# Kernel optimization log

Hardware: AMD Instinct MI355X
Metric: run time of the kernel (lower is better)

Reference implementation:

```python
import math
import jax, jax.numpy as jnp
import numpy as np

B, T, D_MODEL, N_HEADS = 2, 2048, 1024, 16
HEAD_DIM = D_MODEL // N_HEADS  # 64


def setup_inputs() -> dict:
    key = jax.random.key(0)
    k1, k2, k3, k4, k5 = jax.random.split(key, 5)
    x = jax.random.normal(k1, (B, T, D_MODEL), dtype=jnp.float32)
    init = 0.02
    Wq = jax.random.normal(k2, (D_MODEL, D_MODEL), dtype=jnp.float32) * init
    Wk = jax.random.normal(k3, (D_MODEL, D_MODEL), dtype=jnp.float32) * init
    Wv = jax.random.normal(k4, (D_MODEL, D_MODEL), dtype=jnp.float32) * init
    Wo = jax.random.normal(k5, (D_MODEL, D_MODEL), dtype=jnp.float32) * init
    # causal mask, broadcastable over (B, H): 1 = keep, 0 = masked
    mask = jnp.tril(jnp.ones((T, T), dtype=jnp.int32))[None, None, :, :]
    return {"x": x, "Wq": Wq, "Wk": Wk, "Wv": Wv, "Wo": Wo, "mask": mask}


def ternary_weight(W):
    # BitNet-b1.58 style ternary quantization with straight-through estimator
    scale = jnp.mean(jnp.abs(W))
    Wt = jnp.round(jnp.clip(W / (scale + 1e-8), -1.0, 1.0)) * scale
    return W + jax.lax.stop_gradient(Wt - W)


def rope_cos_sin(seq_len, dim):
    inv_freq = 1.0 / (10000.0 ** (jnp.arange(0, dim, 2, dtype=jnp.float32) / dim))
    freqs = jnp.outer(jnp.arange(seq_len, dtype=jnp.float32), inv_freq)  # [T, dim/2]
    emb = jnp.concatenate([freqs, freqs], axis=-1)  # [T, dim]
    return jnp.cos(emb)[None, None, :, :], jnp.sin(emb)[None, None, :, :]


def rotate_half(x):
    h = x.shape[-1] // 2
    return jnp.concatenate([-x[..., h:], x[..., :h]], axis=-1)


def reference(x, Wq, Wk, Wv, Wo, mask):
    Bb, Tt, C = x.shape
    H, D = N_HEADS, HEAD_DIM
    # ternary-quantized projections (bias-free)
    q = (x @ ternary_weight(Wq).T).reshape(Bb, Tt, H, D).transpose(0, 2, 1, 3)
    k = (x @ ternary_weight(Wk).T).reshape(Bb, Tt, H, D).transpose(0, 2, 1, 3)
    v = (x @ ternary_weight(Wv).T).reshape(Bb, Tt, H, D).transpose(0, 2, 1, 3)
    cos, sin = rope_cos_sin(Tt, D)  # [1,1,T,D]
    q = q * cos + rotate_half(q) * sin
    k = k * cos + rotate_half(k) * sin
    att = jnp.einsum("bhqd,bhkd->bhqk", q, k) / math.sqrt(D)
    att = jnp.where(mask == 0, -jnp.inf, att)
    att = jax.nn.softmax(att, axis=-1)  # dropout omitted (eval mode, p effectively 0)
    y = jnp.einsum("bhqk,bhkd->bhqd", att, v)
    y = y.transpose(0, 2, 1, 3).reshape(Bb, Tt, C)
    return y @ ternary_weight(Wo).T
```

## Files before the change

### kernel.cpp

```cpp
#include <hip/hip_runtime.h>
#include <math.h>

using bf16x8  = __attribute__((ext_vector_type(8))) __bf16;
using floatx4 = __attribute__((ext_vector_type(4))) float;
using ushortx8 = __attribute__((ext_vector_type(8))) unsigned short;
typedef unsigned short u16;

__device__ __forceinline__ float bf2f(u16 u) {
  unsigned int x = ((unsigned int)u) << 16;
  return __builtin_bit_cast(float, x);
}
__device__ __forceinline__ u16 f2bf(float f) {
  unsigned int x = __builtin_bit_cast(unsigned int, f);
  x += 0x7FFFu + ((x >> 16) & 1u);
  return (u16)(x >> 16);
}
__device__ __forceinline__ float fexp2(float x) { return __builtin_amdgcn_exp2f(x); }
__device__ __forceinline__ unsigned cvtpk(float lo, float hi) {
  unsigned r;
  asm("v_cvt_pk_bf16_f32 %0, %1, %2" : "=v"(r) : "v"(lo), "v"(hi));
  return r;
}

__global__ __launch_bounds__(256) void cvt_kernel(const float* __restrict__ x, u16* __restrict__ xb) {
  int g = (blockIdx.x * 256 + threadIdx.x) * 8;
  float4 a = *(const float4*)(x + g);
  float4 b = *(const float4*)(x + g + 4);
  ushortx8 o;
  o[0] = f2bf(a.x); o[1] = f2bf(a.y); o[2] = f2bf(a.z); o[3] = f2bf(a.w);
  o[4] = f2bf(b.x); o[5] = f2bf(b.y); o[6] = f2bf(b.z); o[7] = f2bf(b.w);
  *(ushortx8*)(xb + g) = o;
}

__global__ __launch_bounds__(256) void absum_kernel(const float* W0, const float* W1,
                                                    const float* W2, const float* W3,
                                                    float* partials) {
  const float* W = (blockIdx.y == 0) ? W0 : (blockIdx.y == 1) ? W1 : (blockIdx.y == 2) ? W2 : W3;
  int tid = threadIdx.x;
  int base = blockIdx.x * 16384 + tid;
  float s = 0.f;
#pragma unroll
  for (int i = 0; i < 64; ++i) s += fabsf(W[base + i * 256]);
  __shared__ float red[256];
  red[tid] = s;
  __syncthreads();
  for (int off = 128; off > 0; off >>= 1) {
    if (tid < off) red[tid] += red[tid + off];
    __syncthreads();
  }
  if (tid == 0) partials[blockIdx.y * 64 + blockIdx.x] = red[0];
}

__global__ void scales_kernel(const float* partials, float* scales) {
  int w = threadIdx.x;
  if (w < 4) {
    float s = 0.f;
    for (int i = 0; i < 64; ++i) s += partials[w * 64 + i];
    scales[w] = s * (1.f / 1048576.f);
  }
}

__global__ __launch_bounds__(256) void quant_kernel(const float* W0, const float* W1,
                                                    const float* W2, const float* W3,
                                                    const float* scales, u16* Wt) {
  int w = blockIdx.y;
  const float* W = (w == 0) ? W0 : (w == 1) ? W1 : (w == 2) ? W2 : W3;
  u16* O = Wt + (size_t)w * (1u << 20);
  float s = scales[w] + 1e-8f;
  int e = blockIdx.x * 256 + threadIdx.x;
  float t = W[e] / s;
  t = fminf(fmaxf(t, -1.f), 1.f);
  O[e] = f2bf(rintf(t));
}

__global__ __launch_bounds__(256) void gemm_qkv(const u16* __restrict__ A, const u16* __restrict__ Wt,
                                                u16* __restrict__ QKV, const float* __restrict__ scales) {
  const int K = 1024;
  __shared__ __align__(16) u16 As[128][64];
  __shared__ __align__(16) u16 Bs[128][64];
  int tid = threadIdx.x;
  int wave = tid >> 6, lane = tid & 63;
  int quad = lane >> 4, l16 = lane & 15;
  int bm = blockIdx.x * 128;
  int bnc = blockIdx.y * 128;
  int mat = bnc >> 10, bn = bnc & 1023;
  int wm = (wave >> 1) * 64, wn = (wave & 1) * 64;
  floatx4 acc[4][4] = {};
  const u16* ga = A  + (size_t)(bm + wave * 32 + (lane >> 3)) * K + (lane & 7) * 8;
  const u16* gb = Wt + (size_t)(bnc + wave * 32 + (lane >> 3)) * K + (lane & 7) * 8;
  for (int k0 = 0; k0 < K; k0 += 64) {
    __syncthreads();
#pragma unroll
    for (int i = 0; i < 4; ++i)
      __builtin_amdgcn_global_load_lds(
          (const __attribute__((address_space(1))) void*)(ga + (size_t)i * 8 * K + k0),
          (__attribute__((address_space(3))) void*)(&As[wave * 32 + i * 8][0]), 16, 0, 0);
#pragma unroll
    for (int i = 0; i < 4; ++i)
      __builtin_amdgcn_global_load_lds(
          (const __attribute__((address_space(1))) void*)(gb + (size_t)i * 8 * K + k0),
          (__attribute__((address_space(3))) void*)(&Bs[wave * 32 + i * 8][0]), 16, 0, 0);
    __syncthreads();
#pragma unroll
    for (int kk = 0; kk < 64; kk += 32) {
      bf16x8 a[4], b[4];
#pragma unroll
      for (int i = 0; i < 4; ++i)
        a[i] = __builtin_bit_cast(bf16x8, *(const ushortx8*)&As[wm + i * 16 + l16][kk + quad * 8]);
#pragma unroll
      for (int j = 0; j < 4; ++j)
        b[j] = __builtin_bit_cast(bf16x8, *(const ushortx8*)&Bs[wn + j * 16 + l16][kk + quad * 8]);
#pragma unroll
      for (int i = 0; i < 4; ++i)
#pragma unroll
        for (int j = 0; j < 4; ++j)
          acc[i][j] = __builtin_amdgcn_mfma_f32_16x16x32_bf16(a[i], b[j], acc[i][j], 0, 0, 0);
    }
  }
  float sc = scales[mat];
  u16* out = QKV + (size_t)mat * (4u << 20);
#pragma unroll
  for (int i = 0; i < 4; ++i)
#pragma unroll
    for (int j = 0; j < 4; ++j)
#pragma unroll
      for (int rg = 0; rg < 4; ++rg) {
        int row = bm + wm + i * 16 + quad * 4 + rg;
        int col = bn + wn + j * 16 + l16;
        out[(size_t)row * 1024 + col] = f2bf(acc[i][j][rg] * sc);
      }
}

__global__ __launch_bounds__(256) void gemm_out(const u16* __restrict__ A, const u16* __restrict__ B,
                                                float* __restrict__ C, const float* __restrict__ scale_ptr) {
  const int K = 1024, N = 1024;
  __shared__ __align__(16) u16 As[128][64];
  __shared__ __align__(16) u16 Bs[128][64];
  int tid = threadIdx.x;
  int wave = tid >> 6, lane = tid & 63;
  int quad = lane >> 4, l16 = lane & 15;
  int bm = blockIdx.x * 128, bn = blockIdx.y * 128;
  int wm = (wave >> 1) * 64, wn = (wave & 1) * 64;
  floatx4 acc[4][4] = {};
  const u16* ga = A + (size_t)(bm + wave * 32 + (lane >> 3)) * K + (lane & 7) * 8;
  const u16* gb = B + (size_t)(bn + wave * 32 + (lane >> 3)) * K + (lane & 7) * 8;
  for (int k0 = 0; k0 < K; k0 += 64) {
    __syncthreads();
#pragma unroll
    for (int i = 0; i < 4; ++i)
      __builtin_amdgcn_global_load_lds(
          (const __attribute__((address_space(1))) void*)(ga + (size_t)i * 8 * K + k0),
          (__attribute__((address_space(3))) void*)(&As[wave * 32 + i * 8][0]), 16, 0, 0);
#pragma unroll
    for (int i = 0; i < 4; ++i)
      __builtin_amdgcn_global_load_lds(
          (const __attribute__((address_space(1))) void*)(gb + (size_t)i * 8 * K + k0),
          (__attribute__((address_space(3))) void*)(&Bs[wave * 32 + i * 8][0]), 16, 0, 0);
    __syncthreads();
#pragma unroll
    for (int kk = 0; kk < 64; kk += 32) {
      bf16x8 a[4], b[4];
#pragma unroll
      for (int i = 0; i < 4; ++i)
        a[i] = __builtin_bit_cast(bf16x8, *(const ushortx8*)&As[wm + i * 16 + l16][kk + quad * 8]);
#pragma unroll
      for (int j = 0; j < 4; ++j)
        b[j] = __builtin_bit_cast(bf16x8, *(const ushortx8*)&Bs[wn + j * 16 + l16][kk + quad * 8]);
#pragma unroll
      for (int i = 0; i < 4; ++i)
#pragma unroll
        for (int j = 0; j < 4; ++j)
          acc[i][j] = __builtin_amdgcn_mfma_f32_16x16x32_bf16(a[i], b[j], acc[i][j], 0, 0, 0);
    }
  }
  float sc = scale_ptr[0];
#pragma unroll
  for (int i = 0; i < 4; ++i)
#pragma unroll
    for (int j = 0; j < 4; ++j)
#pragma unroll
      for (int rg = 0; rg < 4; ++rg) {
        int row = bm + wm + i * 16 + quad * 4 + rg;
        int col = bn + wn + j * 16 + l16;
        C[(size_t)row * N + col] = acc[i][j][rg] * sc;
      }
}

__global__ __launch_bounds__(256) void rope_kernel(u16* q, u16* k) {
  const float QS = 0.125f * 1.4426950408889634f;
  int gid = blockIdx.x * 256 + threadIdx.x;
  int i = gid & 31;
  int h = (gid >> 5) & 15;
  int bt = gid >> 9;
  int t = bt & 2047;
  float inv = exp2f(-(float)i * (13.287712379549449f / 32.f));
  float ang = (float)t * inv;
  float s = __sinf(ang), c = __cosf(ang);
  int row = bt * 1024 + h * 64;
  float q1 = bf2f(q[row + i]), q2 = bf2f(q[row + i + 32]);
  q[row + i]      = f2bf((q1 * c - q2 * s) * QS);
  q[row + i + 32] = f2bf((q2 * c + q1 * s) * QS);
  float k1 = bf2f(k[row + i]), k2 = bf2f(k[row + i + 32]);
  k[row + i]      = f2bf(k1 * c - k2 * s);
  k[row + i + 32] = f2bf(k2 * c + k1 * s);
}

__global__ __launch_bounds__(256) void vtrans_kernel(const u16* __restrict__ v, u16* __restrict__ vt) {
  __shared__ u16 L[64][66];
  int bh = blockIdx.y, b = bh >> 4, h = bh & 15;
  int t0 = blockIdx.x * 64;
  int tid = threadIdx.x;
  int r = tid >> 2, c = (tid & 3) << 4;
  const u16* src = v + (size_t)(b * 2048 + t0 + r) * 1024 + h * 64 + c;
  *(ushortx8*)&L[r][c]     = *(const ushortx8*)src;
  *(ushortx8*)&L[r][c + 8] = *(const ushortx8*)(src + 8);
  __syncthreads();
  int d = tid >> 2, tc = (tid & 3) << 4;
  ushortx8 o0, o1;
#pragma unroll
  for (int j = 0; j < 8; ++j) { o0[j] = L[tc + j][d]; o1[j] = L[tc + 8 + j][d]; }
  u16* dst = vt + (size_t)(bh * 64 + d) * 2048 + t0 + tc;
  *(ushortx8*)dst       = o0;
  *(ushortx8*)(dst + 8) = o1;
}

__global__ __launch_bounds__(256, 2) void attn_kernel(const u16* __restrict__ q, const u16* __restrict__ k,
                                                      const u16* __restrict__ vt, u16* __restrict__ y) {
  __shared__ __align__(16) u16 Ks[2][64][72];
  __shared__ __align__(16) u16 Vt[2][64][72];
  __shared__ __align__(16) u16 Ps[8][16][72];
  const int T = 2048, C = 1024;
  int tid = threadIdx.x;
  int wave = tid >> 6, lane = tid & 63;
  int quad = lane >> 4, l16 = lane & 15;
  int p = blockIdx.x;
  int b = blockIdx.y >> 4, h = blockIdx.y & 15;
  int wq[2];
  wq[0] = p * 64 + wave * 16;
  wq[1] = (31 - p) * 64 + wave * 16;
  int dt[2] = {p, 31 - p};
  int nkt = 32 - p;

  bf16x8 bq[2][2];
#pragma unroll
  for (int g = 0; g < 2; ++g) {
    const u16* gq = q + (size_t)(b * T + wq[g] + l16) * C + h * 64 + quad * 8;
    bq[g][0] = __builtin_bit_cast(bf16x8, *(const ushortx8*)(gq));
    bq[g][1] = __builtin_bit_cast(bf16x8, *(const ushortx8*)(gq + 32));
  }

  ushortx8 onesu;
#pragma unroll
  for (int j = 0; j < 8; ++j) onesu[j] = 0x3F80;
  bf16x8 bones = __builtin_bit_cast(bf16x8, onesu);

  int srow = tid >> 2, sc16 = (tid & 3) << 4;
  const u16* kptr  = k  + (size_t)(b * T + srow) * C + h * 64 + sc16;
  const u16* vtptr = vt + (size_t)(blockIdx.y * 64 + srow) * 2048 + sc16;

  floatx4 o[2][5] = {};

  ushortx8 kra = *(const ushortx8*)kptr;
  ushortx8 krb = *(const ushortx8*)(kptr + 8);
  ushortx8 vra = *(const ushortx8*)vtptr;
  ushortx8 vrb = *(const ushortx8*)(vtptr + 8);
  *(ushortx8*)&Ks[0][srow][sc16]     = kra;
  *(ushortx8*)&Ks[0][srow][sc16 + 8] = krb;
  *(ushortx8*)&Vt[0][srow][sc16]     = vra;
  *(ushortx8*)&Vt[0][srow][sc16 + 8] = vrb;
  __syncthreads();

  for (int kt = 0; kt < nkt; ++kt) {
    int cur = kt & 1;
    bool haveNext = (kt + 1) < nkt;
    if (haveNext) {
      kra = *(const ushortx8*)(kptr + (size_t)(kt + 1) * 64 * C);
      krb = *(const ushortx8*)(kptr + (size_t)(kt + 1) * 64 * C + 8);
      vra = *(const ushortx8*)(vtptr + (kt + 1) * 64);
      vrb = *(const ushortx8*)(vtptr + (kt + 1) * 64 + 8);
    }

    bool act[2] = {kt <= dt[0], true};

    floatx4 sacc[2][4] = {};
#pragma unroll
    for (int nt = 0; nt < 4; ++nt) {
      bf16x8 ak0 = __builtin_bit_cast(bf16x8, *(const ushortx8*)&Ks[cur][nt * 16 + l16][quad * 8]);
      bf16x8 ak1 = __builtin_bit_cast(bf16x8, *(const ushortx8*)&Ks[cur][nt * 16 + l16][32 + quad * 8]);
#pragma unroll
      for (int g = 0; g < 2; ++g)
        if (act[g]) {
          sacc[g][nt] = __builtin_amdgcn_mfma_f32_16x16x32_bf16(ak0, bq[g][0], sacc[g][nt], 0, 0, 0);
          sacc[g][nt] = __builtin_amdgcn_mfma_f32_16x16x32_bf16(ak1, bq[g][1], sacc[g][nt], 0, 0, 0);
        }
    }

#pragma unroll
    for (int g = 0; g < 2; ++g)
      if (act[g]) {
        if (kt == dt[g]) {
          int qg = wq[g] + l16;
#pragma unroll
          for (int nt = 0; nt < 4; ++nt)
#pragma unroll
            for (int rg = 0; rg < 4; ++rg)
              if (kt * 64 + nt * 16 + quad * 4 + rg > qg) sacc[g][nt][rg] = -__builtin_inff();
        }
#pragma unroll
        for (int nt = 0; nt < 4; ++nt) {
          float p0 = fexp2(sacc[g][nt][0]);
          float p1 = fexp2(sacc[g][nt][1]);
          float p2 = fexp2(sacc[g][nt][2]);
          float p3 = fexp2(sacc[g][nt][3]);
          unsigned lo = cvtpk(p0, p1);
          unsigned hi = cvtpk(p2, p3);
          *(uint2*)&Ps[wave * 2 + g][l16][nt * 16 + quad * 4] = make_uint2(lo, hi);
        }
      }

    bf16x8 ap[2][2];
#pragma unroll
    for (int g = 0; g < 2; ++g)
      if (act[g]) {
        ap[g][0] = __builtin_bit_cast(bf16x8, *(const ushortx8*)&Ps[wave * 2 + g][l16][quad * 8]);
        ap[g][1] = __builtin_bit_cast(bf16x8, *(const ushortx8*)&Ps[wave * 2 + g][l16][32 + quad * 8]);
      }
#pragma unroll
    for (int nt = 0; nt < 4; ++nt) {
      bf16x8 bv0 = __builtin_bit_cast(bf16x8, *(const ushortx8*)&Vt[cur][nt * 16 + l16][quad * 8]);
      bf16x8 bv1 = __builtin_bit_cast(bf16x8, *(const ushortx8*)&Vt[cur][nt * 16 + l16][32 + quad * 8]);
#pragma unroll
      for (int g = 0; g < 2; ++g)
        if (act[g]) {
          o[g][nt] = __builtin_amdgcn_mfma_f32_16x16x32_bf16(ap[g][0], bv0, o[g][nt], 0, 0, 0);
          o[g][nt] = __builtin_amdgcn_mfma_f32_16x16x32_bf16(ap[g][1], bv1, o[g][nt], 0, 0, 0);
        }
    }
#pragma unroll
    for (int g = 0; g < 2; ++g)
      if (act[g]) {
        o[g][4] = __builtin_amdgcn_mfma_f32_16x16x32_bf16(ap[g][0], bones, o[g][4], 0, 0, 0);
        o[g][4] = __builtin_amdgcn_mfma_f32_16x16x32_bf16(ap[g][1], bones, o[g][4], 0, 0, 0);
      }

    if (haveNext) {
      int nb = cur ^ 1;
      *(ushortx8*)&Ks[nb][srow][sc16]     = kra;
      *(ushortx8*)&Ks[nb][srow][sc16 + 8] = krb;
      *(ushortx8*)&Vt[nb][srow][sc16]     = vra;
      *(ushortx8*)&Vt[nb][srow][sc16 + 8] = vrb;
    }
    __syncthreads();
  }

#pragma unroll
  for (int g = 0; g < 2; ++g)
#pragma unroll
    for (int nt = 0; nt < 4; ++nt)
#pragma unroll
      for (int rg = 0; rg < 4; ++rg) {
        int qg = wq[g] + quad * 4 + rg;
        int col = h * 64 + nt * 16 + l16;
        y[(size_t)(b * T + qg) * C + col] = f2bf(o[g][nt][rg] / o[g][4][rg]);
      }
}

extern "C" void kernel_launch(void* const* d_in, const int* in_sizes, int n_in,
                              void* d_out, int out_size, void* d_ws, size_t ws_size,
                              hipStream_t stream) {
  const float* x  = (const float*)d_in[0];
  const float* Wq = (const float*)d_in[1];
  const float* Wk = (const float*)d_in[2];
  const float* Wv = (const float*)d_in[3];
  const float* Wo = (const float*)d_in[4];

  char* ws = (char*)d_ws;
  float* partials = (float*)ws;
  float* scales   = (float*)(ws + 1024);
  u16* Wt  = (u16*)(ws + 4096);
  u16* xb  = (u16*)(ws + 4096 + (size_t)(8u << 20));
  u16* qb  = xb + (4u << 20);
  u16* kb  = qb + (4u << 20);
  u16* vb  = kb + (4u << 20);
  u16* vtb = vb + (4u << 20);
  u16* yb  = vtb + (4u << 20);
  float* out = (float*)d_out;

  cvt_kernel<<<2048, 256, 0, stream>>>(x, xb);
  absum_kernel<<<dim3(64, 4), 256, 0, stream>>>(Wq, Wk, Wv, Wo, partials);
  scales_kernel<<<1, 64, 0, stream>>>(partials, scales);
  quant_kernel<<<dim3(4096, 4), 256, 0, stream>>>(Wq, Wk, Wv, Wo, scales, Wt);

  gemm_qkv<<<dim3(32, 24), 256, 0, stream>>>(xb, Wt, qb, scales);
  rope_kernel<<<8192, 256, 0, stream>>>(qb, kb);
  vtrans_kernel<<<dim3(32, 32), 256, 0, stream>>>(vb, vtb);
  attn_kernel<<<dim3(16, 32), 256, 0, stream>>>(qb, kb, vtb, yb);
  gemm_out<<<dim3(32, 8), 256, 0, stream>>>(yb, Wt + 3 * (1u << 20), out, scales + 3);
}
```

Before: 227.1 us.

## Fuse RoPE into QKV GEMM epilogue, double-buffer and swizzle GEMM LDS tiles

The RoPE rotation and the Q scaling move into the QKV GEMM epilogue. Each wave's 64-column tile covers one full head, so element pairs (d, d+32) sit in the accumulators j and j+2. This removes the separate rope kernel and its read-modify-write pass over Q and K. Both GEMMs switch to a BK=32 double-buffered LDS pipeline with XOR-swizzled columns to cut bank conflicts and overlap loads with MFMA. The output GEMM tile is halved to 128x64 so the grid has 512 blocks for better occupancy, at the cost of less data reuse per block.

```diff
diff --git a/kernel.cpp b/kernel.cpp
--- a/kernel.cpp
+++ b/kernel.cpp
@@ -76,8 +76,8 @@
 __global__ __launch_bounds__(256) void gemm_qkv(const u16* __restrict__ A, const u16* __restrict__ Wt,
                                                 u16* __restrict__ QKV, const float* __restrict__ scales) {
   const int K = 1024;
-  __shared__ __align__(16) u16 As[128][64];
-  __shared__ __align__(16) u16 Bs[128][64];
+  __shared__ __align__(16) u16 As[2][128][32];
+  __shared__ __align__(16) u16 Bs[2][128][32];
   int tid = threadIdx.x;
   int wave = tid >> 6, lane = tid & 63;
   int quad = lane >> 4, l16 = lane & 15;
@@ -86,123 +86,153 @@
   int mat = bnc >> 10, bn = bnc & 1023;
   int wm = (wave >> 1) * 64, wn = (wave & 1) * 64;
   floatx4 acc[4][4] = {};
-  const u16* ga = A  + (size_t)(bm + wave * 32 + (lane >> 3)) * K + (lane & 7) * 8;
-  const u16* gb = Wt + (size_t)(bnc + wave * 32 + (lane >> 3)) * K + (lane & 7) * 8;
-  for (int k0 = 0; k0 < K; k0 += 64) {
+  int srow = wave * 16 + (lane >> 2);
+  int scol = ((lane & 3) ^ ((lane >> 3) & 3)) * 8;
+  const u16* ga = A  + (size_t)(bm + srow) * K + scol;
+  const u16* gb = Wt + (size_t)(bnc + srow) * K + scol;
+  int rca = (quad ^ ((l16 >> 1) & 3)) * 8;
+
+#pragma unroll
+  for (int i = 0; i < 2; ++i) {
+    __builtin_amdgcn_global_load_lds(
+        (const __attribute__((address_space(1))) void*)(ga + (size_t)i * 64 * K),
+        (__attribute__((address_space(3))) void*)(&As[0][i * 64 + wave * 16][0]), 16, 0, 0);
+    __builtin_amdgcn_global_load_lds(
+        (const __attribute__((address_space(1))) void*)(gb + (size_t)i * 64 * K),
+        (__attribute__((address_space(3))) void*)(&Bs[0][i * 64 + wave * 16][0]), 16, 0, 0);
+  }
+  __syncthreads();
+
+  for (int k0 = 0; k0 < K; k0 += 32) {
+    int cur = (k0 >> 5) & 1;
+    if (k0 + 32 < K) {
+      int nb = cur ^ 1;
+#pragma unroll
+      for (int i = 0; i < 2; ++i) {
+        __builtin_amdgcn_global_load_lds(
+            (const __attribute__((address_space(1))) void*)(ga + (size_t)i * 64 * K + k0 + 32),
+            (__attribute__((address_space(3))) void*)(&As[nb][i * 64 + wave * 16][0]), 16, 0, 0);
+        __builtin_amdgcn_global_load_lds(
+            (const __attribute__((address_space(1))) void*)(gb + (size_t)i * 64 * K + k0 + 32),
+            (__attribute__((address_space(3))) void*)(&Bs[nb][i * 64 + wave * 16][0]), 16, 0, 0);
+      }
+    }
+    bf16x8 a[4], b[4];
+#pragma unroll
+    for (int i = 0; i < 4; ++i)
+      a[i] = __builtin_bit_cast(bf16x8, *(const ushortx8*)&As[cur][wm + i * 16 + l16][rca]);
+#pragma unroll
+    for (int j = 0; j < 4; ++j)
+      b[j] = __builtin_bit_cast(bf16x8, *(const ushortx8*)&Bs[cur][wn + j * 16 + l16][rca]);
+#pragma unroll
+    for (int i = 0; i < 4; ++i)
+#pragma unroll
+      for (int j = 0; j < 4; ++j)
+        acc[i][j] = __builtin_amdgcn_mfma_f32_16x16x32_bf16(a[i], b[j], acc[i][j], 0, 0, 0);
     __syncthreads();
-#pragma unroll
-    for (int i = 0; i < 4; ++i)
-      __builtin_amdgcn_global_load_lds(
-          (const __attribute__((address_space(1))) void*)(ga + (size_t)i * 8 * K + k0),
-          (__attribute__((address_space(3))) void*)(&As[wave * 32 + i * 8][0]), 16, 0, 0);
-#pragma unroll
-    for (int i = 0; i < 4; ++i)
-      __builtin_amdgcn_global_load_lds(
-          (const __attribute__((address_space(1))) void*)(gb + (size_t)i * 8 * K + k0),
-          (__attribute__((address_space(3))) void*)(&Bs[wave * 32 + i * 8][0]), 16, 0, 0);
-    __syncthreads();
-#pragma unroll
-    for (int kk = 0; kk < 64; kk += 32) {
-      bf16x8 a[4], b[4];
-#pragma unroll
-      for (int i = 0; i < 4; ++i)
-        a[i] = __builtin_bit_cast(bf16x8, *(const ushortx8*)&As[wm + i * 16 + l16][kk + quad * 8]);
-#pragma unroll
-      for (int j = 0; j < 4; ++j)
-        b[j] = __builtin_bit_cast(bf16x8, *(const ushortx8*)&Bs[wn + j * 16 + l16][kk + quad * 8]);
-#pragma unroll
-      for (int i = 0; i < 4; ++i)
-#pragma unroll
-        for (int j = 0; j < 4; ++j)
-          acc[i][j] = __builtin_amdgcn_mfma_f32_16x16x32_bf16(a[i], b[j], acc[i][j], 0, 0, 0);
-    }
-  }
+  }
+
   float sc = scales[mat];
   u16* out = QKV + (size_t)mat * (4u << 20);
-#pragma unroll
-  for (int i = 0; i < 4; ++i)
-#pragma unroll
-    for (int j = 0; j < 4; ++j)
+  if (mat < 2) {
+    float qs = (mat == 0) ? 0.125f * 1.4426950408889634f : 1.0f;
+    float inv0 = exp2f(-(float)l16 * (13.287712379549449f / 32.f));
+    float inv1 = exp2f(-(float)(16 + l16) * (13.287712379549449f / 32.f));
+#pragma unroll
+    for (int i = 0; i < 4; ++i)
 #pragma unroll
       for (int rg = 0; rg < 4; ++rg) {
         int row = bm + wm + i * 16 + quad * 4 + rg;
-        int col = bn + wn + j * 16 + l16;
-        out[(size_t)row * 1024 + col] = f2bf(acc[i][j][rg] * sc);
-      }
+        float tf = (float)(row & 2047);
+#pragma unroll
+        for (int j = 0; j < 2; ++j) {
+          float ang = tf * (j ? inv1 : inv0);
+          float s = __sinf(ang), c = __cosf(ang);
+          float v1 = acc[i][j][rg] * sc, v2 = acc[i][j + 2][rg] * sc;
+          int col = bn + wn + j * 16 + l16;
+          out[(size_t)row * 1024 + col]      = f2bf((v1 * c - v2 * s) * qs);
+          out[(size_t)row * 1024 + col + 32] = f2bf((v2 * c + v1 * s) * qs);
+        }
+      }
+  } else {
+#pragma unroll
+    for (int i = 0; i < 4; ++i)
+#pragma unroll
+      for (int j = 0; j < 4; ++j)
+#pragma unroll
+        for (int rg = 0; rg < 4; ++rg) {
+          int row = bm + wm + i * 16 + quad * 4 + rg;
+          int col = bn + wn + j * 16 + l16;
+          out[(size_t)row * 1024 + col] = f2bf(acc[i][j][rg] * sc);
+        }
+  }
 }
 
 __global__ __launch_bounds__(256) void gemm_out(const u16* __restrict__ A, const u16* __restrict__ B,
                                                 float* __restrict__ C, const float* __restrict__ scale_ptr) {
   const int K = 1024, N = 1024;
-  __shared__ __align__(16) u16 As[128][64];
-  __shared__ __align__(16) u16 Bs[128][64];
+  __shared__ __align__(16) u16 As[2][128][32];
+  __shared__ __align__(16) u16 Bs[2][64][32];
   int tid = threadIdx.x;
   int wave = tid >> 6, lane = tid & 63;
   int quad = lane >> 4, l16 = lane & 15;
-  int bm = blockIdx.x * 128, bn = blockIdx.y * 128;
-  int wm = (wave >> 1) * 64, wn = (wave & 1) * 64;
-  floatx4 acc[4][4] = {};
-  const u16* ga = A + (size_t)(bm + wave * 32 + (lane >> 3)) * K + (lane & 7) * 8;
-  const u16* gb = B + (size_t)(bn + wave * 32 + (lane >> 3)) * K + (lane & 7) * 8;
-  for (int k0 = 0; k0 < K; k0 += 64) {
+  int bm = blockIdx.x * 128, bn = blockIdx.y * 64;
+  int wm = (wave >> 1) * 64, wn = (wave & 1) * 32;
+  floatx4 acc[4][2] = {};
+  int srow = wave * 16 + (lane >> 2);
+  int scol = ((lane & 3) ^ ((lane >> 3) & 3)) * 8;
+  const u16* ga = A + (size_t)(bm + srow) * K + scol;
+  const u16* gb = B + (size_t)(bn + srow) * K + scol;
+  int rca = (quad ^ ((l16 >> 1) & 3)) * 8;
+
+#pragma unroll
+  for (int i = 0; i < 2; ++i)
+    __builtin_amdgcn_global_load_lds(
+        (const __attribute__((address_space(1))) void*)(ga + (size_t)i * 64 * K),
+        (__attribute__((address_space(3))) void*)(&As[0][i * 64 + wave * 16][0]), 16, 0, 0);
+  __builtin_amdgcn_global_load_lds(
+      (const __attribute__((address_space(1))) void*)(gb),
+      (__attribute__((address_space(3))) void*)(&Bs[0][wave * 16][0]), 16, 0, 0);
+  __syncthreads();
+
+  for (int k0 = 0; k0 < K; k0 += 32) {
+    int cur = (k0 >> 5) & 1;
+    if (k0 + 32 < K) {
+      int nb = cur ^ 1;
+#pragma unroll
+      for (int i = 0; i < 2; ++i)
+        __builtin_amdgcn_global_load_lds(
+            (const __attribute__((address_space(1))) void*)(ga + (size_t)i * 64 * K + k0 + 32),
+            (__attribute__((address_space(3))) void*)(&As[nb][i * 64 + wave * 16][0]), 16, 0, 0);
+      __builtin_amdgcn_global_load_lds(
+          (const __attribute__((address_space(1))) void*)(gb + k0 + 32),
+          (__attribute__((address_space(3))) void*)(&Bs[nb][wave * 16][0]), 16, 0, 0);
+    }
+    bf16x8 a[4], b[2];
+#pragma unroll
+    for (int i = 0; i < 4; ++i)
+      a[i] = __builtin_bit_cast(bf16x8, *(const ushortx8*)&As[cur][wm + i * 16 + l16][rca]);
+#pragma unroll
+    for (int j = 0; j < 2; ++j)
+      b[j] = __builtin_bit_cast(bf16x8, *(const ushortx8*)&Bs[cur][wn + j * 16 + l16][rca]);
+#pragma unroll
+    for (int i = 0; i < 4; ++i)
+#pragma unroll
+      for (int j = 0; j < 2; ++j)
+        acc[i][j] = __builtin_amdgcn_mfma_f32_16x16x32_bf16(a[i], b[j], acc[i][j], 0, 0, 0);
     __syncthreads();
-#pragma unroll
-    for (int i = 0; i < 4; ++i)
-      __builtin_amdgcn_global_load_lds(
-          (const __attribute__((address_space(1))) void*)(ga + (size_t)i * 8 * K + k0),
-          (__attribute__((address_space(3))) void*)(&As[wave * 32 + i * 8][0]), 16, 0, 0);
-#pragma unroll
-    for (int i = 0; i < 4; ++i)
-      __builtin_amdgcn_global_load_lds(
-          (const __attribute__((address_space(1))) void*)(gb + (size_t)i * 8 * K + k0),
-          (__attribute__((address_space(3))) void*)(&Bs[wave * 32 + i * 8][0]), 16, 0, 0);
-    __syncthreads();
-#pragma unroll
-    for (int kk = 0; kk < 64; kk += 32) {
-      bf16x8 a[4], b[4];
-#pragma unroll
-      for (int i = 0; i < 4; ++i)
-        a[i] = __builtin_bit_cast(bf16x8, *(const ushortx8*)&As[wm + i * 16 + l16][kk + quad * 8]);
-#pragma unroll
-      for (int j = 0; j < 4; ++j)
-        b[j] = __builtin_bit_cast(bf16x8, *(const ushortx8*)&Bs[wn + j * 16 + l16][kk + quad * 8]);
-#pragma unroll
-      for (int i = 0; i < 4; ++i)
-#pragma unroll
-        for (int j = 0; j < 4; ++j)
-          acc[i][j] = __builtin_amdgcn_mfma_f32_16x16x32_bf16(a[i], b[j], acc[i][j], 0, 0, 0);
-    }
   }
   float sc = scale_ptr[0];
 #pragma unroll
   for (int i = 0; i < 4; ++i)
 #pragma unroll
-    for (int j = 0; j < 4; ++j)
+    for (int j = 0; j < 2; ++j)
 #pragma unroll
       for (int rg = 0; rg < 4; ++rg) {
         int row = bm + wm + i * 16 + quad * 4 + rg;
         int col = bn + wn + j * 16 + l16;
         C[(size_t)row * N + col] = acc[i][j][rg] * sc;
       }
-}
-
-__global__ __launch_bounds__(256) void rope_kernel(u16* q, u16* k) {
-  const float QS = 0.125f * 1.4426950408889634f;
-  int gid = blockIdx.x * 256 + threadIdx.x;
-  int i = gid & 31;
-  int h = (gid >> 5) & 15;
-  int bt = gid >> 9;
-  int t = bt & 2047;
-  float inv = exp2f(-(float)i * (13.287712379549449f / 32.f));
-  float ang = (float)t * inv;
-  float s = __sinf(ang), c = __cosf(ang);
-  int row = bt * 1024 + h * 64;
-  float q1 = bf2f(q[row + i]), q2 = bf2f(q[row + i + 32]);
-  q[row + i]      = f2bf((q1 * c - q2 * s) * QS);
-  q[row + i + 32] = f2bf((q2 * c + q1 * s) * QS);
-  float k1 = bf2f(k[row + i]), k2 = bf2f(k[row + i + 32]);
-  k[row + i]      = f2bf(k1 * c - k2 * s);
-  k[row + i + 32] = f2bf(k2 * c + k1 * s);
 }
 
 __global__ __launch_bounds__(256) void vtrans_kernel(const u16* __restrict__ v, u16* __restrict__ vt) {
@@ -392,8 +422,7 @@
   quant_kernel<<<dim3(4096, 4), 256, 0, stream>>>(Wq, Wk, Wv, Wo, scales, Wt);
 
   gemm_qkv<<<dim3(32, 24), 256, 0, stream>>>(xb, Wt, qb, scales);
-  rope_kernel<<<8192, 256, 0, stream>>>(qb, kb);
   vtrans_kernel<<<dim3(32, 32), 256, 0, stream>>>(vb, vtb);
   attn_kernel<<<dim3(16, 32), 256, 0, stream>>>(qb, kb, vtb, yb);
-  gemm_out<<<dim3(32, 8), 256, 0, stream>>>(yb, Wt + 3 * (1u << 20), out, scales + 3);
-}
+  gemm_out<<<dim3(32, 16), 256, 0, stream>>>(yb, Wt + 3 * (1u << 20), out, scales + 3);
+}
```

Result: no change. 224.5 us (-1.1%).

## Rewrite QKV GEMM as 256x256 pipelined tile kernel and fuse RoPE epilogue

Applied to the files above, without the earlier changes.

The QKV projection GEMM becomes a 512-thread, 256x256-tile kernel. It double-buffers swizzled LDS tiles, interleaves global-to-LDS prefetch with MFMA phases using barriers and priority hints, and applies RoPE plus the q scaling directly in the epilogue. This lets the separate rope kernel and its extra read/write pass over Q and K be removed. The aim is better latency hiding and fewer bank conflicts in the dominant GEMM. The cost is a launch of only 192 blocks with heavier register and LDS use, plus a more fragile hand-tuned schedule.

```diff
diff --git a/kernel.cpp b/kernel.cpp
--- a/kernel.cpp
+++ b/kernel.cpp
@@ -21,6 +21,10 @@
   asm("v_cvt_pk_bf16_f32 %0, %1, %2" : "=v"(r) : "v"(lo), "v"(hi));
   return r;
 }
+
+#define GLDS16(SRC, DST)                                                        \
+  __builtin_amdgcn_global_load_lds((const __attribute__((address_space(1))) void*)(SRC), \
+                                   (__attribute__((address_space(3))) void*)(DST), 16, 0, 0)
 
 __global__ __launch_bounds__(256) void cvt_kernel(const float* __restrict__ x, u16* __restrict__ xb) {
   int g = (blockIdx.x * 256 + threadIdx.x) * 8;
@@ -73,62 +77,132 @@
   O[e] = f2bf(rintf(t));
 }
 
-__global__ __launch_bounds__(256) void gemm_qkv(const u16* __restrict__ A, const u16* __restrict__ Wt,
-                                                u16* __restrict__ QKV, const float* __restrict__ scales) {
-  const int K = 1024;
-  __shared__ __align__(16) u16 As[128][64];
-  __shared__ __align__(16) u16 Bs[128][64];
+__global__ __launch_bounds__(512, 2) void gemm_qkv(const u16* __restrict__ A, const u16* __restrict__ Wt,
+                                                   u16* __restrict__ QKV, const float* __restrict__ scales) {
+  const int K = 1024, NT = 16;
+  __shared__ __align__(16) u16 Ab[2][2][128][64];
+  __shared__ __align__(16) u16 Bb[2][2][128][64];
   int tid = threadIdx.x;
-  int wave = tid >> 6, lane = tid & 63;
+  int w = tid >> 6, lane = tid & 63;
   int quad = lane >> 4, l16 = lane & 15;
-  int bm = blockIdx.x * 128;
-  int bnc = blockIdx.y * 128;
+  int bm = blockIdx.x * 256;
+  int bnc = blockIdx.y * 256;
+  int halfA = w >> 2;
+  int halfB = (w & 3) >> 1;
+  int cbase = (w & 1) * 64;
+
+  int srow = w * 8 + (lane >> 3);
+  int scol = ((lane & 7) ^ (lane >> 3)) * 8;
+  const u16* gA = A  + (size_t)(bm  + srow) * K + scol;
+  const u16* gB = Wt + (size_t)(bnc + srow) * K + scol;
+
+#define STAGE(BUF, GP, PAR, HF, TAU)                                                    \
+  do {                                                                                  \
+    GLDS16(GP + (size_t)((HF) * 128) * 1024 + (size_t)(TAU) * 64, &BUF[PAR][HF][w * 8][0]); \
+    GLDS16(GP + (size_t)((HF) * 128 + 64) * 1024 + (size_t)(TAU) * 64, &BUF[PAR][HF][64 + w * 8][0]); \
+  } while (0)
+
+  floatx4 acc[8][4] = {};
+
+  STAGE(Ab, gA, 0, 0, 0); STAGE(Ab, gA, 0, 1, 0);
+  STAGE(Bb, gB, 0, 0, 0); STAGE(Bb, gB, 0, 1, 0);
+  STAGE(Bb, gB, 1, 0, 1); STAGE(Bb, gB, 1, 1, 1);
+  asm volatile("s_waitcnt vmcnt(4)" ::: "memory");
+  __builtin_amdgcn_s_barrier();
+
+  for (int it = 0; it < 8; ++it) {
+    int t = it * 2;
+    bf16x8 afr[4][2], bfr[2][2][2];
+#pragma unroll
+    for (int p = 0; p < 8; ++p) {
+      const int qd = p & 3, rh = qd >> 1, ch = qd & 1;
+      const int bb = (p >> 2) & 1;
+      if (ch == 0) {
+#pragma unroll
+        for (int i = 0; i < 4; ++i)
+#pragma unroll
+          for (int kk = 0; kk < 2; ++kk)
+            afr[i][kk] = __builtin_bit_cast(
+                bf16x8, *(const ushortx8*)&Ab[bb][halfA][rh * 64 + i * 16 + l16]
+                                             [((quad + kk * 4) ^ (l16 & 7)) * 8]);
+      }
+      if (rh == 0) {
+#pragma unroll
+        for (int gg = 0; gg < 2; ++gg)
+#pragma unroll
+          for (int kk = 0; kk < 2; ++kk)
+            bfr[ch][gg][kk] = __builtin_bit_cast(
+                bf16x8, *(const ushortx8*)&Bb[bb][halfB][cbase + ch * 32 + gg * 16 + l16]
+                                             [((quad + kk * 4) ^ (l16 & 7)) * 8]);
+      }
+      if (p == 0)      { STAGE(Ab, gA, 1, 0, t + 1); }
+      else if (p == 1) { STAGE(Ab, gA, 1, 1, t + 1); }
+      else if (p == 2) { if (it < 7) STAGE(Bb, gB, 0, 0, t + 2); }
+      else if (p == 3) { if (it < 7) STAGE(Bb, gB, 0, 1, t + 2); }
+      else if (p == 4) { if (it < 7) STAGE(Ab, gA, 0, 0, t + 2); }
+      else if (p == 5) { if (it < 7) STAGE(Ab, gA, 0, 1, t + 2); }
+      else if (p == 6) { if (it < 7) STAGE(Bb, gB, 1, 0, t + 3); }
+      else             { if (it < 7) STAGE(Bb, gB, 1, 1, t + 3); }
+
+      __builtin_amdgcn_s_barrier();
+      asm volatile("s_waitcnt lgkmcnt(0)" ::: "memory");
+      __builtin_amdgcn_sched_barrier(0);
+      __builtin_amdgcn_s_setprio(1);
+#pragma unroll
+      for (int i = 0; i < 4; ++i)
+#pragma unroll
+        for (int gg = 0; gg < 2; ++gg) {
+          acc[rh * 4 + i][ch * 2 + gg] = __builtin_amdgcn_mfma_f32_16x16x32_bf16(
+              afr[i][0], bfr[ch][gg][0], acc[rh * 4 + i][ch * 2 + gg], 0, 0, 0);
+          acc[rh * 4 + i][ch * 2 + gg] = __builtin_amdgcn_mfma_f32_16x16x32_bf16(
+              afr[i][1], bfr[ch][gg][1], acc[rh * 4 + i][ch * 2 + gg], 0, 0, 0);
+        }
+      __builtin_amdgcn_s_setprio(0);
+      if (qd == 3) {
+        if (it < 7) asm volatile("s_waitcnt vmcnt(4)" ::: "memory");
+        else        asm volatile("s_waitcnt vmcnt(0)" ::: "memory");
+      }
+      __builtin_amdgcn_s_barrier();
+      __builtin_amdgcn_sched_barrier(0);
+    }
+  }
+#undef STAGE
+
   int mat = bnc >> 10, bn = bnc & 1023;
-  int wm = (wave >> 1) * 64, wn = (wave & 1) * 64;
-  floatx4 acc[4][4] = {};
-  const u16* ga = A  + (size_t)(bm + wave * 32 + (lane >> 3)) * K + (lane & 7) * 8;
-  const u16* gb = Wt + (size_t)(bnc + wave * 32 + (lane >> 3)) * K + (lane & 7) * 8;
-  for (int k0 = 0; k0 < K; k0 += 64) {
-    __syncthreads();
-#pragma unroll
-    for (int i = 0; i < 4; ++i)
-      __builtin_amdgcn_global_load_lds(
-          (const __attribute__((address_space(1))) void*)(ga + (size_t)i * 8 * K + k0),
-          (__attribute__((address_space(3))) void*)(&As[wave * 32 + i * 8][0]), 16, 0, 0);
-#pragma unroll
-    for (int i = 0; i < 4; ++i)
-      __builtin_amdgcn_global_load_lds(
-          (const __attribute__((address_space(1))) void*)(gb + (size_t)i * 8 * K + k0),
-          (__attribute__((address_space(3))) void*)(&Bs[wave * 32 + i * 8][0]), 16, 0, 0);
-    __syncthreads();
-#pragma unroll
-    for (int kk = 0; kk < 64; kk += 32) {
-      bf16x8 a[4], b[4];
-#pragma unroll
-      for (int i = 0; i < 4; ++i)
-        a[i] = __builtin_bit_cast(bf16x8, *(const ushortx8*)&As[wm + i * 16 + l16][kk + quad * 8]);
-#pragma unroll
-      for (int j = 0; j < 4; ++j)
-        b[j] = __builtin_bit_cast(bf16x8, *(const ushortx8*)&Bs[wn + j * 16 + l16][kk + quad * 8]);
-#pragma unroll
-      for (int i = 0; i < 4; ++i)
-#pragma unroll
-        for (int j = 0; j < 4; ++j)
-          acc[i][j] = __builtin_amdgcn_mfma_f32_16x16x32_bf16(a[i], b[j], acc[i][j], 0, 0, 0);
-    }
-  }
   float sc = scales[mat];
-  u16* out = QKV + (size_t)mat * (4u << 20);
-#pragma unroll
-  for (int i = 0; i < 4; ++i)
-#pragma unroll
-    for (int j = 0; j < 4; ++j)
+  u16* outp = QKV + (size_t)mat * (4u << 20);
+  if (mat < 2) {
+    float qs = (mat == 0) ? 0.125f * 1.4426950408889634f : 1.0f;
+    float inv0 = exp2f(-(float)l16 * (13.287712379549449f / 32.f));
+    float inv1 = exp2f(-(float)(16 + l16) * (13.287712379549449f / 32.f));
+#pragma unroll
+    for (int f = 0; f < 8; ++f)
 #pragma unroll
       for (int rg = 0; rg < 4; ++rg) {
-        int row = bm + wm + i * 16 + quad * 4 + rg;
-        int col = bn + wn + j * 16 + l16;
-        out[(size_t)row * 1024 + col] = f2bf(acc[i][j][rg] * sc);
-      }
+        int row = bm + halfA * 128 + f * 16 + quad * 4 + rg;
+        float tf = (float)(row & 2047);
+#pragma unroll
+        for (int j = 0; j < 2; ++j) {
+          float ang = tf * (j ? inv1 : inv0);
+          float s = __sinf(ang), c = __cosf(ang);
+          float v1 = acc[f][j][rg] * sc, v2 = acc[f][j + 2][rg] * sc;
+          int col = bn + (w & 3) * 64 + j * 16 + l16;
+          outp[(size_t)row * 1024 + col]      = f2bf((v1 * c - v2 * s) * qs);
+          outp[(size_t)row * 1024 + col + 32] = f2bf((v2 * c + v1 * s) * qs);
+        }
+      }
+  } else {
+#pragma unroll
+    for (int f = 0; f < 8; ++f)
+#pragma unroll
+      for (int g = 0; g < 4; ++g)
+#pragma unroll
+        for (int rg = 0; rg < 4; ++rg) {
+          int row = bm + halfA * 128 + f * 16 + quad * 4 + rg;
+          int col = bn + (w & 3) * 64 + g * 16 + l16;
+          outp[(size_t)row * 1024 + col] = f2bf(acc[f][g][rg] * sc);
+        }
+  }
 }
 
 __global__ __launch_bounds__(256) void gemm_out(const u16* __restrict__ A, const u16* __restrict__ B,
@@ -148,14 +222,10 @@
     __syncthreads();
 #pragma unroll
     for (int i = 0; i < 4; ++i)
-      __builtin_amdgcn_global_load_lds(
-          (const __attribute__((address_space(1))) void*)(ga + (size_t)i * 8 * K + k0),
-          (__attribute__((address_space(3))) void*)(&As[wave * 32 + i * 8][0]), 16, 0, 0);
+      GLDS16(ga + (size_t)i * 8 * K + k0, &As[wave * 32 + i * 8][0]);
 #pragma unroll
     for (int i = 0; i < 4; ++i)
-      __builtin_amdgcn_global_load_lds(
-          (const __attribute__((address_space(1))) void*)(gb + (size_t)i * 8 * K + k0),
-          (__attribute__((address_space(3))) void*)(&Bs[wave * 32 + i * 8][0]), 16, 0, 0);
+      GLDS16(gb + (size_t)i * 8 * K + k0, &Bs[wave * 32 + i * 8][0]);
     __syncthreads();
 #pragma unroll
     for (int kk = 0; kk < 64; kk += 32) {
@@ -184,25 +254,6 @@
         int col = bn + wn + j * 16 + l16;
         C[(size_t)row * N + col] = acc[i][j][rg] * sc;
       }
-}
-
-__global__ __launch_bounds__(256) void rope_kernel(u16* q, u16* k) {
-  const float QS = 0.125f * 1.4426950408889634f;
-  int gid = blockIdx.x * 256 + threadIdx.x;
-  int i = gid & 31;
-  int h = (gid >> 5) & 15;
-  int bt = gid >> 9;
-  int t = bt & 2047;
-  float inv = exp2f(-(float)i * (13.287712379549449f / 32.f));
-  float ang = (float)t * inv;
-  float s = __sinf(ang), c = __cosf(ang);
-  int row = bt * 1024 + h * 64;
-  float q1 = bf2f(q[row + i]), q2 = bf2f(q[row + i + 32]);
-  q[row + i]      = f2bf((q1 * c - q2 * s) * QS);
-  q[row + i + 32] = f2bf((q2 * c + q1 * s) * QS);
-  float k1 = bf2f(k[row + i]), k2 = bf2f(k[row + i + 32]);
-  k[row + i]      = f2bf(k1 * c - k2 * s);
-  k[row + i + 32] = f2bf(k2 * c + k1 * s);
 }
 
 __global__ __launch_bounds__(256) void vtrans_kernel(const u16* __restrict__ v, u16* __restrict__ vt) {
@@ -391,8 +442,7 @@
   scales_kernel<<<1, 64, 0, stream>>>(partials, scales);
   quant_kernel<<<dim3(4096, 4), 256, 0, stream>>>(Wq, Wk, Wv, Wo, scales, Wt);
 
-  gemm_qkv<<<dim3(32, 24), 256, 0, stream>>>(xb, Wt, qb, scales);
-  rope_kernel<<<8192, 256, 0, stream>>>(qb, kb);
+  gemm_qkv<<<dim3(16, 12), 512, 0, stream>>>(xb, Wt, qb, scales);
   vtrans_kernel<<<dim3(32, 32), 256, 0, stream>>>(vb, vtb);
   attn_kernel<<<dim3(16, 32), 256, 0, stream>>>(qb, kb, vtb, yb);
   gemm_out<<<dim3(32, 8), 256, 0, stream>>>(yb, Wt + 3 * (1u << 20), out, scales + 3);
```

Result: faster. 212.8 us (-6.3%).

## Fuse RoPE and V transpose into QKV GEMM epilogue, vectorize quantization

Applied to the files above, without the earlier changes.

The QKV GEMM tile changes to 128x64 so that each block covers exactly one head. RoPE rotation and the Q scaling are then applied in the epilogue, and V is written directly in transposed layout. This removes the separate rope and vtrans kernels along with their global memory round trips. The block index is swizzled for L2 locality, and the quant kernel is vectorized to four elements per thread. In exchange, the epilogue does more per-element math and the transposed V stores are narrower.

```diff
diff --git a/kernel.cpp b/kernel.cpp
--- a/kernel.cpp
+++ b/kernel.cpp
@@ -4,6 +4,7 @@
 using bf16x8  = __attribute__((ext_vector_type(8))) __bf16;
 using floatx4 = __attribute__((ext_vector_type(4))) float;
 using ushortx8 = __attribute__((ext_vector_type(8))) unsigned short;
+using ushortx4 = __attribute__((ext_vector_type(4))) unsigned short;
 typedef unsigned short u16;
 
 __device__ __forceinline__ float bf2f(u16 u) {
@@ -21,6 +22,10 @@
   asm("v_cvt_pk_bf16_f32 %0, %1, %2" : "=v"(r) : "v"(lo), "v"(hi));
   return r;
 }
+
+#define GLDS16(SRC, DST)                                                        \
+  __builtin_amdgcn_global_load_lds((const __attribute__((address_space(1))) void*)(SRC), \
+                                   (__attribute__((address_space(3))) void*)(DST), 16, 0, 0)
 
 __global__ __launch_bounds__(256) void cvt_kernel(const float* __restrict__ x, u16* __restrict__ xb) {
   int g = (blockIdx.x * 256 + threadIdx.x) * 8;
@@ -67,68 +72,98 @@
   const float* W = (w == 0) ? W0 : (w == 1) ? W1 : (w == 2) ? W2 : W3;
   u16* O = Wt + (size_t)w * (1u << 20);
   float s = scales[w] + 1e-8f;
-  int e = blockIdx.x * 256 + threadIdx.x;
-  float t = W[e] / s;
-  t = fminf(fmaxf(t, -1.f), 1.f);
-  O[e] = f2bf(rintf(t));
+  int e = (blockIdx.x * 256 + threadIdx.x) * 4;
+  float4 v = *(const float4*)(W + e);
+  ushortx4 o;
+  o[0] = f2bf(rintf(fminf(fmaxf(v.x / s, -1.f), 1.f)));
+  o[1] = f2bf(rintf(fminf(fmaxf(v.y / s, -1.f), 1.f)));
+  o[2] = f2bf(rintf(fminf(fmaxf(v.z / s, -1.f), 1.f)));
+  o[3] = f2bf(rintf(fminf(fmaxf(v.w / s, -1.f), 1.f)));
+  *(ushortx4*)(O + e) = o;
 }
 
 __global__ __launch_bounds__(256) void gemm_qkv(const u16* __restrict__ A, const u16* __restrict__ Wt,
-                                                u16* __restrict__ QKV, const float* __restrict__ scales) {
+                                                u16* __restrict__ QKV, u16* __restrict__ vt,
+                                                const float* __restrict__ scales) {
   const int K = 1024;
   __shared__ __align__(16) u16 As[128][64];
-  __shared__ __align__(16) u16 Bs[128][64];
+  __shared__ __align__(16) u16 Bs[64][64];
   int tid = threadIdx.x;
   int wave = tid >> 6, lane = tid & 63;
   int quad = lane >> 4, l16 = lane & 15;
-  int bm = blockIdx.x * 128;
-  int bnc = blockIdx.y * 128;
+  int flat = blockIdx.y * 32 + blockIdx.x;
+  int swz = (flat & 7) * 192 + (flat >> 3);
+  int bx = swz & 31, by = swz >> 5;
+  int bm = bx * 128;
+  int bnc = by * 64;
   int mat = bnc >> 10, bn = bnc & 1023;
-  int wm = (wave >> 1) * 64, wn = (wave & 1) * 64;
-  floatx4 acc[4][4] = {};
+  int wm = wave * 32;
+  floatx4 acc[2][4] = {};
   const u16* ga = A  + (size_t)(bm + wave * 32 + (lane >> 3)) * K + (lane & 7) * 8;
-  const u16* gb = Wt + (size_t)(bnc + wave * 32 + (lane >> 3)) * K + (lane & 7) * 8;
+  const u16* gb = Wt + (size_t)(bnc + wave * 16 + (lane >> 3)) * K + (lane & 7) * 8;
   for (int k0 = 0; k0 < K; k0 += 64) {
     __syncthreads();
 #pragma unroll
     for (int i = 0; i < 4; ++i)
-      __builtin_amdgcn_global_load_lds(
-          (const __attribute__((address_space(1))) void*)(ga + (size_t)i * 8 * K + k0),
-          (__attribute__((address_space(3))) void*)(&As[wave * 32 + i * 8][0]), 16, 0, 0);
-#pragma unroll
-    for (int i = 0; i < 4; ++i)
-      __builtin_amdgcn_global_load_lds(
-          (const __attribute__((address_space(1))) void*)(gb + (size_t)i * 8 * K + k0),
-          (__attribute__((address_space(3))) void*)(&Bs[wave * 32 + i * 8][0]), 16, 0, 0);
+      GLDS16(ga + (size_t)i * 8 * K + k0, &As[wave * 32 + i * 8][0]);
+#pragma unroll
+    for (int i = 0; i < 2; ++i)
+      GLDS16(gb + (size_t)i * 8 * K + k0, &Bs[wave * 16 + i * 8][0]);
     __syncthreads();
 #pragma unroll
     for (int kk = 0; kk < 64; kk += 32) {
-      bf16x8 a[4], b[4];
-#pragma unroll
-      for (int i = 0; i < 4; ++i)
+      bf16x8 a[2], b[4];
+#pragma unroll
+      for (int i = 0; i < 2; ++i)
         a[i] = __builtin_bit_cast(bf16x8, *(const ushortx8*)&As[wm + i * 16 + l16][kk + quad * 8]);
 #pragma unroll
       for (int j = 0; j < 4; ++j)
-        b[j] = __builtin_bit_cast(bf16x8, *(const ushortx8*)&Bs[wn + j * 16 + l16][kk + quad * 8]);
-#pragma unroll
-      for (int i = 0; i < 4; ++i)
+        b[j] = __builtin_bit_cast(bf16x8, *(const ushortx8*)&Bs[j * 16 + l16][kk + quad * 8]);
+#pragma unroll
+      for (int i = 0; i < 2; ++i)
 #pragma unroll
         for (int j = 0; j < 4; ++j)
           acc[i][j] = __builtin_amdgcn_mfma_f32_16x16x32_bf16(a[i], b[j], acc[i][j], 0, 0, 0);
     }
   }
   float sc = scales[mat];
-  u16* out = QKV + (size_t)mat * (4u << 20);
-#pragma unroll
-  for (int i = 0; i < 4; ++i)
-#pragma unroll
-    for (int j = 0; j < 4; ++j)
+  if (mat < 2) {
+    u16* outp = QKV + (size_t)mat * (4u << 20);
+    float qs = (mat == 0) ? 0.125f * 1.4426950408889634f : 1.0f;
+    float inv0 = exp2f(-(float)l16 * (13.287712379549449f / 32.f));
+    float inv1 = exp2f(-(float)(16 + l16) * (13.287712379549449f / 32.f));
+#pragma unroll
+    for (int i = 0; i < 2; ++i)
 #pragma unroll
       for (int rg = 0; rg < 4; ++rg) {
         int row = bm + wm + i * 16 + quad * 4 + rg;
-        int col = bn + wn + j * 16 + l16;
-        out[(size_t)row * 1024 + col] = f2bf(acc[i][j][rg] * sc);
-      }
+        float tf = (float)(row & 2047);
+#pragma unroll
+        for (int j = 0; j < 2; ++j) {
+          float ang = tf * (j ? inv1 : inv0);
+          float s = __sinf(ang), c = __cosf(ang);
+          float v1 = acc[i][j][rg] * sc, v2 = acc[i][j + 2][rg] * sc;
+          int col = bn + j * 16 + l16;
+          outp[(size_t)row * 1024 + col]      = f2bf((v1 * c - v2 * s) * qs);
+          outp[(size_t)row * 1024 + col + 32] = f2bf((v2 * c + v1 * s) * qs);
+        }
+      }
+  } else {
+    int h = bn >> 6;
+#pragma unroll
+    for (int i = 0; i < 2; ++i) {
+      int row0 = bm + wm + i * 16 + quad * 4;
+      int b = row0 >> 11, t0 = row0 & 2047;
+#pragma unroll
+      for (int j = 0; j < 4; ++j) {
+        int d = j * 16 + l16;
+        ushortx4 o;
+#pragma unroll
+        for (int rg = 0; rg < 4; ++rg) o[rg] = f2bf(acc[i][j][rg] * sc);
+        *(ushortx4*)(vt + (size_t)((b * 16 + h) * 64 + d) * 2048 + t0) = o;
+      }
+    }
+  }
 }
 
 __global__ __launch_bounds__(256) void gemm_out(const u16* __restrict__ A, const u16* __restrict__ B,
@@ -148,14 +183,10 @@
     __syncthreads();
 #pragma unroll
     for (int i = 0; i < 4; ++i)
-      __builtin_amdgcn_global_load_lds(
-          (const __attribute__((address_space(1))) void*)(ga + (size_t)i * 8 * K + k0),
-          (__attribute__((address_space(3))) void*)(&As[wave * 32 + i * 8][0]), 16, 0, 0);
+      GLDS16(ga + (size_t)i * 8 * K + k0, &As[wave * 32 + i * 8][0]);
 #pragma unroll
     for (int i = 0; i < 4; ++i)
-      __builtin_amdgcn_global_load_lds(
-          (const __attribute__((address_space(1))) void*)(gb + (size_t)i * 8 * K + k0),
-          (__attribute__((address_space(3))) void*)(&Bs[wave * 32 + i * 8][0]), 16, 0, 0);
+      GLDS16(gb + (size_t)i * 8 * K + k0, &Bs[wave * 32 + i * 8][0]);
     __syncthreads();
 #pragma unroll
     for (int kk = 0; kk < 64; kk += 32) {
@@ -184,44 +215,6 @@
         int col = bn + wn + j * 16 + l16;
         C[(size_t)row * N + col] = acc[i][j][rg] * sc;
       }
-}
-
-__global__ __launch_bounds__(256) void rope_kernel(u16* q, u16* k) {
-  const float QS = 0.125f * 1.4426950408889634f;
-  int gid = blockIdx.x * 256 + threadIdx.x;
-  int i = gid & 31;
-  int h = (gid >> 5) & 15;
-  int bt = gid >> 9;
-  int t = bt & 2047;
-  float inv = exp2f(-(float)i * (13.287712379549449f / 32.f));
-  float ang = (float)t * inv;
-  float s = __sinf(ang), c = __cosf(ang);
-  int row = bt * 1024 + h * 64;
-  float q1 = bf2f(q[row + i]), q2 = bf2f(q[row + i + 32]);
-  q[row + i]      = f2bf((q1 * c - q2 * s) * QS);
-  q[row + i + 32] = f2bf((q2 * c + q1 * s) * QS);
-  float k1 = bf2f(k[row + i]), k2 = bf2f(k[row + i + 32]);
-  k[row + i]      = f2bf(k1 * c - k2 * s);
-  k[row + i + 32] = f2bf(k2 * c + k1 * s);
-}
-
-__global__ __launch_bounds__(256) void vtrans_kernel(const u16* __restrict__ v, u16* __restrict__ vt) {
-  __shared__ u16 L[64][66];
-  int bh = blockIdx.y, b = bh >> 4, h = bh & 15;
-  int t0 = blockIdx.x * 64;
-  int tid = threadIdx.x;
-  int r = tid >> 2, c = (tid & 3) << 4;
-  const u16* src = v + (size_t)(b * 2048 + t0 + r) * 1024 + h * 64 + c;
-  *(ushortx8*)&L[r][c]     = *(const ushortx8*)src;
-  *(ushortx8*)&L[r][c + 8] = *(const ushortx8*)(src + 8);
-  __syncthreads();
-  int d = tid >> 2, tc = (tid & 3) << 4;
-  ushortx8 o0, o1;
-#pragma unroll
-  for (int j = 0; j < 8; ++j) { o0[j] = L[tc + j][d]; o1[j] = L[tc + 8 + j][d]; }
-  u16* dst = vt + (size_t)(bh * 64 + d) * 2048 + t0 + tc;
-  *(ushortx8*)dst       = o0;
-  *(ushortx8*)(dst + 8) = o1;
 }
 
 __global__ __launch_bounds__(256, 2) void attn_kernel(const u16* __restrict__ q, const u16* __restrict__ k,
@@ -381,19 +374,16 @@
   u16* xb  = (u16*)(ws + 4096 + (size_t)(8u << 20));
   u16* qb  = xb + (4u << 20);
   u16* kb  = qb + (4u << 20);
-  u16* vb  = kb + (4u << 20);
-  u16* vtb = vb + (4u << 20);
+  u16* vtb = kb + (4u << 20);
   u16* yb  = vtb + (4u << 20);
   float* out = (float*)d_out;
 
   cvt_kernel<<<2048, 256, 0, stream>>>(x, xb);
   absum_kernel<<<dim3(64, 4), 256, 0, stream>>>(Wq, Wk, Wv, Wo, partials);
   scales_kernel<<<1, 64, 0, stream>>>(partials, scales);
-  quant_kernel<<<dim3(4096, 4), 256, 0, stream>>>(Wq, Wk, Wv, Wo, scales, Wt);
-
-  gemm_qkv<<<dim3(32, 24), 256, 0, stream>>>(xb, Wt, qb, scales);
-  rope_kernel<<<8192, 256, 0, stream>>>(qb, kb);
-  vtrans_kernel<<<dim3(32, 32), 256, 0, stream>>>(vb, vtb);
+  quant_kernel<<<dim3(1024, 4), 256, 0, stream>>>(Wq, Wk, Wv, Wo, scales, Wt);
+
+  gemm_qkv<<<dim3(32, 48), 256, 0, stream>>>(xb, Wt, qb, vtb, scales);
   attn_kernel<<<dim3(16, 32), 256, 0, stream>>>(qb, kb, vtb, yb);
   gemm_out<<<dim3(32, 8), 256, 0, stream>>>(yb, Wt + 3 * (1u << 20), out, scales + 3);
 }
```

Measured after the change: 214.8 us. 5.4% less time.
